# Kernel optimization log

Hardware: AMD Instinct MI355X
Metric: run time of the kernel (lower is better)

The kernel has to match this reference:

```python
import jax, jax.numpy as jnp
import numpy as np

HID = 5120      # hidden_size
QLR = 1536      # q_lora_rank
KVLR = 512      # kv_lora_rank
NOPE = 128      # qk_nope_head_dim
ROPE = 64       # qk_rope_head_dim
VDIM = 128      # v_head_dim
H = 32          # num_local_heads
T = 2048        # tokens (single causal prefill, prefix_len=0)
QKD = NOPE + ROPE
SCALE = QKD ** -0.5
EPS = 1e-6
THETA = 10000.0


def rmsnorm(x, w):
    return x * jax.lax.rsqrt(jnp.mean(x * x, axis=-1, keepdims=True) + EPS) * w


def rope_cos_sin(positions):
    inv_freq = 1.0 / (THETA ** (jnp.arange(0, ROPE, 2, dtype=jnp.float32) / ROPE))
    freqs = positions.astype(jnp.float32)[:, None] * inv_freq  # [T, ROPE/2]
    return jnp.cos(freqs), jnp.sin(freqs)


def apply_rope(x, cos, sin):
    # non-neox (interleaved, GPT-J style) rotation on last dim of size ROPE
    x1 = x[..., ::2]
    x2 = x[..., 1::2]
    o1 = x1 * cos - x2 * sin
    o2 = x2 * cos + x1 * sin
    return jnp.stack([o1, o2], axis=-1).reshape(x.shape)


def setup_inputs() -> dict:
    key = jax.random.key(0)
    ks = jax.random.split(key, 10)
    s = 0.02
    return {
        "hidden_states": jax.random.normal(ks[0], (T, HID), jnp.float32),
        "positions": jnp.arange(T, dtype=jnp.int64),
        "w_q_a": jax.random.normal(ks[1], (HID, QLR), jnp.float32) * s,
        "q_a_ln_w": jnp.ones((QLR,), jnp.float32),
        "w_q_b": jax.random.normal(ks[2], (QLR, H * QKD), jnp.float32) * s,
        "w_kv_a": jax.random.normal(ks[3], (HID, KVLR + ROPE), jnp.float32) * s,
        "kv_a_ln_w": jnp.ones((KVLR,), jnp.float32),
        "w_kc": jax.random.normal(ks[4], (H, NOPE, KVLR), jnp.float32) * s,  # absorbed K weight
        "w_vc": jax.random.normal(ks[5], (H, KVLR, VDIM), jnp.float32) * s,  # absorbed V weight
        "w_o": jax.random.normal(ks[6], (H * VDIM, HID), jnp.float32) * s,
    }


def reference(hidden_states, positions, w_q_a, q_a_ln_w, w_q_b, w_kv_a, kv_a_ln_w, w_kc, w_vc, w_o):
    # --- low-rank Q projection ---
    q = rmsnorm(hidden_states @ w_q_a, q_a_ln_w) @ w_q_b          # [T, H*QKD]
    q = q.reshape(T, H, QKD)
    q_nope, q_pe = q[..., :NOPE], q[..., NOPE:]                   # [T,H,NOPE], [T,H,ROPE]

    # --- absorbed q_nope: project into kv_lora space via w_kc ---
    q_nope_out = jnp.einsum("thd,hdk->thk", q_nope, w_kc)         # [T, H, KVLR]

    # --- latent KV ---
    latent = hidden_states @ w_kv_a                               # [T, KVLR+ROPE]
    v_input = rmsnorm(latent[:, :KVLR], kv_a_ln_w)                # [T, KVLR]
    k_pe = latent[:, KVLR:]                                       # [T, ROPE]

    # --- partial RoPE (non-neox) ---
    cos, sin = rope_cos_sin(positions)                            # [T, ROPE/2]
    q_pe = apply_rope(q_pe, cos[:, None, :], sin[:, None, :])
    k_pe = apply_rope(k_pe, cos, sin)

    q_input = jnp.concatenate([q_nope_out, q_pe], axis=-1)        # [T, H, KVLR+ROPE]
    k_input = jnp.concatenate([v_input, k_pe], axis=-1)           # [T, KVLR+ROPE], shared (MQA)

    # --- causal MQA attention over latent KV ---
    scores = jnp.einsum("thd,sd->hts", q_input, k_input) * SCALE  # [H, T, T]
    causal = jnp.tril(jnp.ones((T, T), dtype=bool))
    scores = jnp.where(causal, scores, -1e30)
    probs = jax.nn.softmax(scores, axis=-1)
    ctx = jnp.einsum("hts,sr->thr", probs, v_input)               # [T, H, KVLR]

    # --- absorbed output projection via w_vc, then o_proj ---
    attn_out = jnp.einsum("thr,hrv->thv", ctx, w_vc).reshape(T, H * VDIM)
    return attn_out @ w_o                                         # [T, HID]
```

## Files before the change

### kernel.cpp

```cpp
#include <hip/hip_runtime.h>

#define T_SEQ 2048
#define HID   5120
#define QLR   1536
#define KVLR  512
#define NOPE  128
#define ROPE_D 64
#define VDIM  128
#define NH    32
#define QKD   192

constexpr float SCALE   = 0.07216878364870323f;
constexpr float EPS_F   = 1e-6f;
constexpr float LN10000 = 9.210340371976184f;

typedef __bf16 bf16x8 __attribute__((ext_vector_type(8)));
typedef float  f32x4  __attribute__((ext_vector_type(4)));

__device__ __forceinline__ unsigned short f2bf(float f) {
  union { float f; unsigned u; } v; v.f = f;
  unsigned u = v.u + 0x7fffu + ((v.u >> 16) & 1u);
  return (unsigned short)(u >> 16);
}
__device__ __forceinline__ float bf2f(unsigned short b) {
  union { unsigned u; float f; } v; v.u = ((unsigned)b) << 16;
  return v.f;
}

__device__ __forceinline__ void glds16(const unsigned short* g, unsigned short* l) {
  __builtin_amdgcn_global_load_lds((const __attribute__((address_space(1))) void*)g,
                                   (__attribute__((address_space(3))) void*)l, 16, 0, 0);
}

__global__ void conv_f2b(const float* __restrict__ in, unsigned short* __restrict__ out, long n) {
  long i = ((long)blockIdx.x * blockDim.x + threadIdx.x) * 4;
  if (i >= n) return;
  float4 v = *(const float4*)(in + i);
  uint2 o;
  o.x = (unsigned)f2bf(v.x) | ((unsigned)f2bf(v.y) << 16);
  o.y = (unsigned)f2bf(v.z) | ((unsigned)f2bf(v.w) << 16);
  *(uint2*)(out + i) = o;
}

__global__ void transpose_f2b(const float* __restrict__ in, unsigned short* __restrict__ out,
                              int R, int C, long inB, long outB) {
  __shared__ float tile[32][33];
  const float* inp = in + (long)blockIdx.z * inB;
  unsigned short* outp = out + (long)blockIdx.z * outB;
  int c0 = blockIdx.x * 32, r0 = blockIdx.y * 32;
  int x = threadIdx.x, y = threadIdx.y;
#pragma unroll
  for (int yy = 0; yy < 32; yy += 8)
    tile[y + yy][x] = inp[(long)(r0 + y + yy) * C + c0 + x];
  __syncthreads();
#pragma unroll
  for (int yy = 0; yy < 32; yy += 8)
    outp[(long)(c0 + y + yy) * R + r0 + x] = f2bf(tile[x][y + yy]);
}

__global__ void rmsnorm_rows(const float* __restrict__ in, const float* __restrict__ w,
                             unsigned short* __restrict__ out, int C) {
  int t = blockIdx.x, tid = threadIdx.x;
  __shared__ float sred[4];
  const float* row = in + (long)t * C;
  float ss = 0.f;
  for (int i = tid; i < C; i += 256) { float v = row[i]; ss += v * v; }
#pragma unroll
  for (int o = 32; o; o >>= 1) ss += __shfl_xor(ss, o);
  if ((tid & 63) == 0) sred[tid >> 6] = ss;
  __syncthreads();
  ss = sred[0] + sred[1] + sred[2] + sred[3];
  float rinv = rsqrtf(ss / (float)C + EPS_F);
  for (int i = tid; i < C; i += 256)
    out[(long)t * C + i] = f2bf(row[i] * rinv * w[i]);
}

__global__ void norm_rope_k(const float* __restrict__ latent, const float* __restrict__ w,
                            unsigned short* __restrict__ k_input, unsigned short* __restrict__ v_t) {
  int t = blockIdx.x, tid = threadIdx.x;
  __shared__ float sred[4];
  const float* row = latent + (long)t * 576;
  float ss = 0.f;
  for (int i = tid; i < 512; i += 256) { float v = row[i]; ss += v * v; }
#pragma unroll
  for (int o = 32; o; o >>= 1) ss += __shfl_xor(ss, o);
  if ((tid & 63) == 0) sred[tid >> 6] = ss;
  __syncthreads();
  ss = sred[0] + sred[1] + sred[2] + sred[3];
  float rinv = rsqrtf(ss * (1.f / 512.f) + EPS_F);
  for (int i = tid; i < 512; i += 256) {
    unsigned short b = f2bf(row[i] * rinv * w[i]);
    k_input[(long)t * 576 + i] = b;
    v_t[(long)i * T_SEQ + t] = b;
  }
  if (tid < 32) {
    float fr = (float)t * expf(-((float)(2 * tid) / 64.f) * LN10000);
    float c = cosf(fr), s = sinf(fr);
    float x1 = row[512 + 2 * tid], x2 = row[512 + 2 * tid + 1];
    k_input[(long)t * 576 + 512 + 2 * tid]     = f2bf(x1 * c - x2 * s);
    k_input[(long)t * 576 + 512 + 2 * tid + 1] = f2bf(x2 * c + x1 * s);
  }
}

__global__ void rope_q(const unsigned short* __restrict__ q, unsigned short* __restrict__ q_input) {
  int idx = blockIdx.x * 256 + threadIdx.x;
  int i = idx & 31, h = (idx >> 5) & 31, t = idx >> 10;
  float fr = (float)t * expf(-((float)(2 * i) / 64.f) * LN10000);
  float c = cosf(fr), s = sinf(fr);
  const unsigned short* qp = q + (long)t * (NH * QKD) + h * QKD + NOPE + 2 * i;
  float x1 = bf2f(qp[0]), x2 = bf2f(qp[1]);
  unsigned short* op = q_input + ((long)h * T_SEQ + t) * 576 + 512 + 2 * i;
  op[0] = f2bf(x1 * c - x2 * s);
  op[1] = f2bf(x2 * c + x1 * s);
}

template <bool OUT_BF16>
__global__ __launch_bounds__(256, 2)
void gemm_bt(const unsigned short* __restrict__ A, const unsigned short* __restrict__ Bt,
             void* __restrict__ Cv, int N, int K,
             long lda, long ldb, long ldc, long bA, long bB, long bC) {
  __shared__ __align__(16) unsigned short sA[128 * 64];
  __shared__ __align__(16) unsigned short sB[128 * 64];
  const int b = blockIdx.z;
  const unsigned short* Ap = A + (long)b * bA;
  const unsigned short* Bp = Bt + (long)b * bB;
  const int m0 = blockIdx.x * 128, n0 = blockIdx.y * 128;
  const int tid = threadIdx.x, lane = tid & 63, w = tid >> 6;
  const int wr = w >> 1, wc = w & 1, lo = lane & 15, hi = lane >> 4;
  f32x4 acc[4][4];
#pragma unroll
  for (int i = 0; i < 4; i++)
#pragma unroll
    for (int j = 0; j < 4; j++) acc[i][j] = (f32x4){0.f, 0.f, 0.f, 0.f};
  const int r0 = tid >> 3, cc = tid & 7;
  for (int k0 = 0; k0 < K; k0 += 64) {
    __syncthreads();
#pragma unroll
    for (int i = 0; i < 4; i++) {
      glds16(Ap + (long)(m0 + i * 32 + r0) * lda + k0 + cc * 8, sA + i * 2048 + w * 512);
      glds16(Bp + (long)(n0 + i * 32 + r0) * ldb + k0 + cc * 8, sB + i * 2048 + w * 512);
    }
    __syncthreads();
#pragma unroll
    for (int s = 0; s < 2; s++) {
      bf16x8 af[4], bfr[4];
#pragma unroll
      for (int mt = 0; mt < 4; mt++)
        af[mt] = *(const bf16x8*)(sA + (wr * 64 + mt * 16 + lo) * 64 + s * 32 + hi * 8);
#pragma unroll
      for (int nt = 0; nt < 4; nt++)
        bfr[nt] = *(const bf16x8*)(sB + (wc * 64 + nt * 16 + lo) * 64 + s * 32 + hi * 8);
#pragma unroll
      for (int mt = 0; mt < 4; mt++)
#pragma unroll
        for (int nt = 0; nt < 4; nt++)
          acc[mt][nt] = __builtin_amdgcn_mfma_f32_16x16x32_bf16(af[mt], bfr[nt], acc[mt][nt], 0, 0, 0);
    }
  }
#pragma unroll
  for (int mt = 0; mt < 4; mt++)
#pragma unroll
    for (int nt = 0; nt < 4; nt++) {
      int col = n0 + wc * 64 + nt * 16 + lo;
      if (col < N) {
#pragma unroll
        for (int r = 0; r < 4; r++) {
          long row = m0 + wr * 64 + mt * 16 + hi * 4 + r;
          float v = acc[mt][nt][r];
          if constexpr (OUT_BF16)
            ((unsigned short*)Cv)[(long)b * bC + row * ldc + col] = f2bf(v);
          else
            ((float*)Cv)[(long)b * bC + row * ldc + col] = v;
        }
      }
    }
}

__global__ __launch_bounds__(256, 2)
void flash_attn(const unsigned short* __restrict__ q_input,
                const unsigned short* __restrict__ k_input,
                const unsigned short* __restrict__ v_t,
                unsigned short* __restrict__ ctx_out) {
  __shared__ __align__(16) unsigned short sK[2 * 64 * 96];
  __shared__ __align__(16) unsigned short sV[2 * 128 * 64];
  const int h = blockIdx.x;
  const int i0 = (31 - blockIdx.y) * 64;
  const int tid = threadIdx.x;
  const int lane = tid & 63, w = tid >> 6;
  const int lo = lane & 15, hi = lane >> 4;
  const int qrow = i0 + w * 16 + lo;

  bf16x8 qf[18];
  {
    const unsigned short* qr = q_input + ((long)h * T_SEQ + qrow) * 576;
#pragma unroll
    for (int i = 0; i < 18; i++) qf[i] = *(const bf16x8*)(qr + i * 32 + hi * 8);
  }
  float l_r = 0.f;
  f32x4 of[32];
#pragma unroll
  for (int o = 0; o < 32; o++) of[o] = (f32x4){0.f, 0.f, 0.f, 0.f};

  int kOff[3];
#pragma unroll
  for (int i = 0; i < 3; i++) {
    int u = w * 192 + i * 64 + lane;
    int key = (u * 683) >> 13;
    int dg = u - 12 * key;
    kOff[i] = key * 576 + dg * 8;
  }
  int vOff[4];
#pragma unroll
  for (int i = 0; i < 4; i++) {
    int u = w * 256 + i * 64 + lane;
    int us = u ^ ((u >> 3) & 7);
    vOff[i] = (u >> 3) * T_SEQ + (us & 7) * 8;
  }
  const int vsw[2] = { ((0 + hi) ^ (lo & 7)) * 8, ((4 + hi) ^ (lo & 7)) * 8 };
  unsigned short* kdst = sK + w * 3 * 512;
  unsigned short* vdst = sV + w * 4 * 512;
  const unsigned short* kld = sK + lo * 96 + hi * 8;
  const unsigned short* vld = sV + lo * 64;

#pragma unroll
  for (int i = 0; i < 3; i++) glds16(k_input + kOff[i], kdst + i * 512);

  for (int j0 = 0; j0 <= i0; j0 += 64) {
    f32x4 sacc[4];
#pragma unroll
    for (int nt = 0; nt < 4; nt++) sacc[nt] = (f32x4){0.f, 0.f, 0.f, 0.f};
#pragma unroll
    for (int c = 0; c < 6; c++) {
      __syncthreads();
      if (c < 5) {
        const int bn = (c + 1) & 1;
#pragma unroll
        for (int i = 0; i < 3; i++)
          glds16(k_input + kOff[i] + (c + 1) * 96, kdst + bn * 6144 + i * 512);
      } else {
#pragma unroll
        for (int i = 0; i < 4; i++) glds16(v_t + vOff[i], vdst + i * 512);
      }
      const unsigned short* kb = kld + (c & 1) * 6144;
#pragma unroll
      for (int ks = 0; ks < 3; ks++)
#pragma unroll
        for (int nt = 0; nt < 4; nt++) {
          bf16x8 a = *(const bf16x8*)(kb + nt * 1536 + ks * 32);
          sacc[nt] = __builtin_amdgcn_mfma_f32_16x16x32_bf16(a, qf[3 * c + ks], sacc[nt], 0, 0, 0);
        }
    }
    const bool diag = (j0 == i0);
    int D2[4][2];
    float psum = 0.f;
#pragma unroll
    for (int nt = 0; nt < 4; nt++) {
      float pv[4];
#pragma unroll
      for (int r = 0; r < 4; r++) {
        float e = __expf(sacc[nt][r] * SCALE);
        if (diag && (j0 + nt * 16 + hi * 4 + r) > qrow) e = 0.f;
        pv[r] = e;
        psum += e;
      }
      D2[nt][0] = (int)f2bf(pv[0]) | ((int)f2bf(pv[1]) << 16);
      D2[nt][1] = (int)f2bf(pv[2]) | ((int)f2bf(pv[3]) << 16);
    }
    psum += __shfl_xor(psum, 16);
    psum += __shfl_xor(psum, 32);
    l_r += psum;
    bf16x8 pa[2];
    {
      const int s0 = lo + 32 * (hi & 1);
#pragma unroll
      for (int kk = 0; kk < 2; kk++) {
        int d[4];
#pragma unroll
        for (int dd = 0; dd < 2; dd++) {
          int t0 = __shfl(D2[2 * kk][dd], s0);
          int t1 = __shfl(D2[2 * kk + 1][dd], s0);
          d[dd] = (hi >> 1) ? t1 : t0;
          int t2 = __shfl(D2[2 * kk][dd], s0 + 16);
          int t3 = __shfl(D2[2 * kk + 1][dd], s0 + 16);
          d[2 + dd] = (hi >> 1) ? t3 : t2;
        }
        int4 di = {d[0], d[1], d[2], d[3]};
        pa[kk] = *(bf16x8*)&di;
      }
    }
#pragma unroll
    for (int ch = 0; ch < 4; ch++) {
      __syncthreads();
      if (ch < 3) {
        const int bn = (ch + 1) & 1;
#pragma unroll
        for (int i = 0; i < 4; i++)
          glds16(v_t + vOff[i] + (ch + 1) * 128 * T_SEQ, vdst + bn * 8192 + i * 512);
      } else {
#pragma unroll
        for (int i = 0; i < 3; i++) kOff[i] += 64 * 576;
#pragma unroll
        for (int i = 0; i < 4; i++) vOff[i] += 64;
        if (j0 < i0) {
#pragma unroll
          for (int i = 0; i < 3; i++) glds16(k_input + kOff[i], kdst + i * 512);
        }
      }
      const unsigned short* vb = vld + (ch & 1) * 8192;
#pragma unroll
      for (int kk = 0; kk < 2; kk++)
#pragma unroll
        for (int ot = 0; ot < 8; ot++) {
          bf16x8 bfr = *(const bf16x8*)(vb + ot * 1024 + vsw[kk]);
          of[ch * 8 + ot] =
              __builtin_amdgcn_mfma_f32_16x16x32_bf16(pa[kk], bfr, of[ch * 8 + ot], 0, 0, 0);
        }
    }
  }
  float linv[4];
#pragma unroll
  for (int r = 0; r < 4; r++) linv[r] = 1.f / __shfl(l_r, hi * 4 + r);
#pragma unroll
  for (int o = 0; o < 32; o++) {
    int vd = (o >> 3) * 128 + (o & 7) * 16 + lo;
#pragma unroll
    for (int r = 0; r < 4; r++) {
      long row = (long)h * T_SEQ + i0 + w * 16 + hi * 4 + r;
      ctx_out[row * 576 + vd] = f2bf(of[o][r] * linv[r]);
    }
  }
}

extern "C" void kernel_launch(void* const* d_in, const int* in_sizes, int n_in,
                              void* d_out, int out_size, void* d_ws, size_t ws_size,
                              hipStream_t stream) {
  (void)in_sizes; (void)n_in; (void)out_size; (void)ws_size;
  const float* hs    = (const float*)d_in[0];
  const float* wqa   = (const float*)d_in[2];
  const float* qlnw  = (const float*)d_in[3];
  const float* wqb   = (const float*)d_in[4];
  const float* wkva  = (const float*)d_in[5];
  const float* kvlnw = (const float*)d_in[6];
  const float* wkc   = (const float*)d_in[7];
  const float* wvc   = (const float*)d_in[8];
  const float* wo    = (const float*)d_in[9];
  float* out = (float*)d_out;

  char* base = (char*)d_ws;
  size_t off = 0;
  auto alloc = [&](size_t bytes) {
    char* r = base + off;
    off += (bytes + 255) & ~(size_t)255;
    return r;
  };
  unsigned short* hs_b  = (unsigned short*)alloc((size_t)T_SEQ * HID * 2);
  unsigned short* wqaT  = (unsigned short*)alloc((size_t)QLR * HID * 2);
  unsigned short* wqbT  = (unsigned short*)alloc((size_t)NH * QKD * QLR * 2);
  unsigned short* wkvaT = (unsigned short*)alloc((size_t)640 * HID * 2);
  unsigned short* wkcT  = (unsigned short*)alloc((size_t)NH * 512 * 128 * 2);
  unsigned short* wvcT  = (unsigned short*)alloc((size_t)NH * 128 * 512 * 2);
  float*          q_a   = (float*)alloc((size_t)T_SEQ * QLR * 4);
  unsigned short* q_a_n = (unsigned short*)alloc((size_t)T_SEQ * QLR * 2);
  unsigned short* qbuf  = (unsigned short*)alloc((size_t)T_SEQ * NH * QKD * 2);
  float*          latent= (float*)alloc((size_t)T_SEQ * 576 * 4);
  unsigned short* k_inp = (unsigned short*)alloc((size_t)T_SEQ * 576 * 2);
  unsigned short* v_t   = (unsigned short*)alloc((size_t)512 * T_SEQ * 2);
  unsigned short* q_inp = (unsigned short*)alloc((size_t)NH * T_SEQ * 576 * 2);
  unsigned short* woT   = (unsigned short*)base;
  unsigned short* attn  = qbuf;

  dim3 tb(32, 8);
  conv_f2b<<<(T_SEQ * HID) / 1024, 256, 0, stream>>>(hs, hs_b, (long)T_SEQ * HID);
  transpose_f2b<<<dim3(QLR / 32, HID / 32, 1), tb, 0, stream>>>(wqa, wqaT, HID, QLR, 0, 0);
  transpose_f2b<<<dim3(576 / 32, HID / 32, 1), tb, 0, stream>>>(wkva, wkvaT, HID, 576, 0, 0);
  gemm_bt<false><<<dim3(T_SEQ / 128, QLR / 128, 1), 256, 0, stream>>>(
      hs_b, wqaT, q_a, QLR, HID, HID, HID, QLR, 0, 0, 0);
  gemm_bt<false><<<dim3(T_SEQ / 128, 5, 1), 256, 0, stream>>>(
      hs_b, wkvaT, latent, 576, HID, HID, HID, 576, 0, 0, 0);
  rmsnorm_rows<<<T_SEQ, 256, 0, stream>>>(q_a, qlnw, q_a_n, QLR);
  norm_rope_k<<<T_SEQ, 256, 0, stream>>>(latent, kvlnw, k_inp, v_t);
  transpose_f2b<<<dim3((NH * QKD) / 32, QLR / 32, 1), tb, 0, stream>>>(wqb, wqbT, QLR, NH * QKD, 0, 0);
  gemm_bt<true><<<dim3(T_SEQ / 128, (NH * QKD) / 128, 1), 256, 0, stream>>>(
      q_a_n, wqbT, qbuf, NH * QKD, QLR, QLR, QLR, NH * QKD, 0, 0, 0);
  transpose_f2b<<<dim3(512 / 32, 128 / 32, NH), tb, 0, stream>>>(wkc, wkcT, 128, 512, 65536, 65536);
  gemm_bt<true><<<dim3(T_SEQ / 128, 512 / 128, NH), 256, 0, stream>>>(
      qbuf, wkcT, q_inp, 512, 128, NH * QKD, 128, 576, QKD, 65536, (long)T_SEQ * 576);
  rope_q<<<(T_SEQ * NH * 32) / 256, 256, 0, stream>>>(qbuf, q_inp);
  flash_attn<<<dim3(NH, 32), 256, 0, stream>>>(q_inp, k_inp, v_t, q_inp);
  transpose_f2b<<<dim3(128 / 32, 512 / 32, NH), tb, 0, stream>>>(wvc, wvcT, 512, 128, 65536, 65536);
  gemm_bt<true><<<dim3(T_SEQ / 128, 1, NH), 256, 0, stream>>>(
      q_inp, wvcT, attn, 128, 512, 576, 512, NH * VDIM, (long)T_SEQ * 576, 65536, 128);
  transpose_f2b<<<dim3(HID / 32, (NH * VDIM) / 32, 1), tb, 0, stream>>>(wo, woT, NH * VDIM, HID, 0, 0);
  gemm_bt<false><<<dim3(T_SEQ / 128, HID / 128, 1), 256, 0, stream>>>(
      attn, woT, out, HID, NH * VDIM, NH * VDIM, NH * VDIM, HID, 0, 0, 0);
}
```

Measured before the change: 1.075 ms.

## Deepen flash-attention K/V staging to a 4-buffer pipeline with explicit vmcnt waits

```diff
diff --git a/kernel.cpp b/kernel.cpp
--- a/kernel.cpp
+++ b/kernel.cpp
@@ -181,8 +181,8 @@
                 const unsigned short* __restrict__ k_input,
                 const unsigned short* __restrict__ v_t,
                 unsigned short* __restrict__ ctx_out) {
-  __shared__ __align__(16) unsigned short sK[2 * 64 * 96];
-  __shared__ __align__(16) unsigned short sV[2 * 128 * 64];
+  __shared__ __align__(16) unsigned short sK[4 * 64 * 64];
+  __shared__ __align__(16) unsigned short sV[4 * 64 * 64];
   const int h = blockIdx.x;
   const int i0 = (31 - blockIdx.y) * 64;
   const int tid = threadIdx.x;
@@ -196,60 +196,92 @@
 #pragma unroll
     for (int i = 0; i < 18; i++) qf[i] = *(const bf16x8*)(qr + i * 32 + hi * 8);
   }
+#pragma unroll
+  for (int i = 0; i < 18; i++) asm volatile("" : "+v"(qf[i]));
+
   float l_r = 0.f;
   f32x4 of[32];
 #pragma unroll
   for (int o = 0; o < 32; o++) of[o] = (f32x4){0.f, 0.f, 0.f, 0.f};
 
-  int kOff[3];
-#pragma unroll
-  for (int i = 0; i < 3; i++) {
-    int u = w * 192 + i * 64 + lane;
-    int key = (u * 683) >> 13;
-    int dg = u - 12 * key;
-    kOff[i] = key * 576 + dg * 8;
-  }
-  int vOff[4];
-#pragma unroll
-  for (int i = 0; i < 4; i++) {
-    int u = w * 256 + i * 64 + lane;
-    int us = u ^ ((u >> 3) & 7);
-    vOff[i] = (u >> 3) * T_SEQ + (us & 7) * 8;
-  }
-  const int vsw[2] = { ((0 + hi) ^ (lo & 7)) * 8, ((4 + hi) ^ (lo & 7)) * 8 };
-  unsigned short* kdst = sK + w * 3 * 512;
-  unsigned short* vdst = sV + w * 4 * 512;
-  const unsigned short* kld = sK + lo * 96 + hi * 8;
+  int kOff[2], vOff[2];
+#pragma unroll
+  for (int i = 0; i < 2; i++) {
+    int u = w * 128 + i * 64 + lane;
+    int sl = (u ^ (u >> 3)) & 7;
+    kOff[i] = (u >> 3) * 576 + sl * 8;
+    vOff[i] = (u >> 3) * T_SEQ + sl * 8;
+  }
+  const int sw[2] = { ((0 + hi) ^ (lo & 7)) * 8, ((4 + hi) ^ (lo & 7)) * 8 };
+  unsigned short* kdst = sK + w * 1024;
+  unsigned short* vdst = sV + w * 1024;
+  const unsigned short* kld = sK + lo * 64;
   const unsigned short* vld = sV + lo * 64;
 
-#pragma unroll
-  for (int i = 0; i < 3; i++) glds16(k_input + kOff[i], kdst + i * 512);
+#define STAGE_K(c, base)                                                      \
+  {                                                                           \
+    unsigned short* d_ = kdst + ((c) & 3) * 4096;                             \
+    _Pragma("unroll")                                                         \
+    for (int i_ = 0; i_ < 2; i_++)                                            \
+      glds16(k_input + (base) + kOff[i_] + (c) * 64, d_ + i_ * 512);          \
+  }
+#define STAGE_V(ch, jk)                                                       \
+  {                                                                           \
+    unsigned short* d_ = vdst + ((ch) & 3) * 4096;                            \
+    _Pragma("unroll")                                                         \
+    for (int i_ = 0; i_ < 2; i_++)                                            \
+      glds16(v_t + (long)(ch) * 64 * T_SEQ + vOff[i_] + (jk), d_ + i_ * 512); \
+  }
+#define WB(N)                                                                 \
+  __builtin_amdgcn_sched_barrier(0);                                          \
+  asm volatile("s_waitcnt vmcnt(" #N ")" ::: "memory");                       \
+  __builtin_amdgcn_s_barrier();                                               \
+  __builtin_amdgcn_sched_barrier(0);
+#define COMPUTE_K(c)                                                          \
+  {                                                                           \
+    const unsigned short* kb_ = kld + ((c) & 3) * 4096;                       \
+    _Pragma("unroll")                                                         \
+    for (int ks_ = 0; ks_ < 2; ks_++)                                         \
+      _Pragma("unroll")                                                       \
+      for (int nt_ = 0; nt_ < 4; nt_++) {                                     \
+        bf16x8 a_ = *(const bf16x8*)(kb_ + nt_ * 1024 + sw[ks_]);             \
+        sacc[nt_] = __builtin_amdgcn_mfma_f32_16x16x32_bf16(                  \
+            a_, qf[2 * (c) + ks_], sacc[nt_], 0, 0, 0);                       \
+      }                                                                       \
+  }
+#define COMPUTE_V(ch)                                                         \
+  {                                                                           \
+    const unsigned short* vb_ = vld + ((ch) & 3) * 4096;                      \
+    _Pragma("unroll")                                                         \
+    for (int kk_ = 0; kk_ < 2; kk_++)                                         \
+      _Pragma("unroll")                                                       \
+      for (int ot_ = 0; ot_ < 4; ot_++) {                                     \
+        bf16x8 b_ = *(const bf16x8*)(vb_ + ot_ * 1024 + sw[kk_]);             \
+        of[(ch) * 4 + ot_] = __builtin_amdgcn_mfma_f32_16x16x32_bf16(         \
+            pa[kk_], b_, of[(ch) * 4 + ot_], 0, 0, 0);                        \
+      }                                                                       \
+  }
+
+  STAGE_K(0, 0); STAGE_K(1, 0);
 
   for (int j0 = 0; j0 <= i0; j0 += 64) {
+    const long kcur = (long)j0 * 576;
+    const long knxt = kcur + 64 * 576;
+    const bool more = (j0 < i0);
     f32x4 sacc[4];
 #pragma unroll
     for (int nt = 0; nt < 4; nt++) sacc[nt] = (f32x4){0.f, 0.f, 0.f, 0.f};
-#pragma unroll
-    for (int c = 0; c < 6; c++) {
-      __syncthreads();
-      if (c < 5) {
-        const int bn = (c + 1) & 1;
-#pragma unroll
-        for (int i = 0; i < 3; i++)
-          glds16(k_input + kOff[i] + (c + 1) * 96, kdst + bn * 6144 + i * 512);
-      } else {
-#pragma unroll
-        for (int i = 0; i < 4; i++) glds16(v_t + vOff[i], vdst + i * 512);
-      }
-      const unsigned short* kb = kld + (c & 1) * 6144;
-#pragma unroll
-      for (int ks = 0; ks < 3; ks++)
-#pragma unroll
-        for (int nt = 0; nt < 4; nt++) {
-          bf16x8 a = *(const bf16x8*)(kb + nt * 1536 + ks * 32);
-          sacc[nt] = __builtin_amdgcn_mfma_f32_16x16x32_bf16(a, qf[3 * c + ks], sacc[nt], 0, 0, 0);
-        }
-    }
+
+    STAGE_K(2, kcur); WB(4); COMPUTE_K(0);
+    STAGE_K(3, kcur); WB(4); COMPUTE_K(1);
+    STAGE_K(4, kcur); WB(4); COMPUTE_K(2);
+    STAGE_K(5, kcur); WB(4); COMPUTE_K(3);
+    STAGE_K(6, kcur); WB(4); COMPUTE_K(4);
+    STAGE_K(7, kcur); WB(4); COMPUTE_K(5);
+    STAGE_K(8, kcur); WB(4); COMPUTE_K(6);
+    STAGE_V(0, j0);   WB(4); COMPUTE_K(7);
+    STAGE_V(1, j0);   WB(4); COMPUTE_K(8);
+
     const bool diag = (j0 == i0);
     int D2[4][2];
     float psum = 0.f;
@@ -288,41 +320,29 @@
         pa[kk] = *(bf16x8*)&di;
       }
     }
-#pragma unroll
-    for (int ch = 0; ch < 4; ch++) {
-      __syncthreads();
-      if (ch < 3) {
-        const int bn = (ch + 1) & 1;
-#pragma unroll
-        for (int i = 0; i < 4; i++)
-          glds16(v_t + vOff[i] + (ch + 1) * 128 * T_SEQ, vdst + bn * 8192 + i * 512);
-      } else {
-#pragma unroll
-        for (int i = 0; i < 3; i++) kOff[i] += 64 * 576;
-#pragma unroll
-        for (int i = 0; i < 4; i++) vOff[i] += 64;
-        if (j0 < i0) {
-#pragma unroll
-          for (int i = 0; i < 3; i++) glds16(k_input + kOff[i], kdst + i * 512);
-        }
-      }
-      const unsigned short* vb = vld + (ch & 1) * 8192;
-#pragma unroll
-      for (int kk = 0; kk < 2; kk++)
-#pragma unroll
-        for (int ot = 0; ot < 8; ot++) {
-          bf16x8 bfr = *(const bf16x8*)(vb + ot * 1024 + vsw[kk]);
-          of[ch * 8 + ot] =
-              __builtin_amdgcn_mfma_f32_16x16x32_bf16(pa[kk], bfr, of[ch * 8 + ot], 0, 0, 0);
-        }
-    }
-  }
+    STAGE_V(2, j0); WB(4); COMPUTE_V(0);
+    STAGE_V(3, j0); WB(4); COMPUTE_V(1);
+    STAGE_V(4, j0); WB(4); COMPUTE_V(2);
+    STAGE_V(5, j0); WB(4); COMPUTE_V(3);
+    STAGE_V(6, j0); WB(4); COMPUTE_V(4);
+    STAGE_V(7, j0); WB(4); COMPUTE_V(5);
+    if (more) { STAGE_K(0, knxt); WB(4); } else { WB(2); }
+    COMPUTE_V(6);
+    if (more) { STAGE_K(1, knxt); WB(4); } else { WB(0); }
+    COMPUTE_V(7);
+  }
+#undef STAGE_K
+#undef STAGE_V
+#undef WB
+#undef COMPUTE_K
+#undef COMPUTE_V
+
   float linv[4];
 #pragma unroll
   for (int r = 0; r < 4; r++) linv[r] = 1.f / __shfl(l_r, hi * 4 + r);
 #pragma unroll
   for (int o = 0; o < 32; o++) {
-    int vd = (o >> 3) * 128 + (o & 7) * 16 + lo;
+    int vd = o * 16 + lo;
 #pragma unroll
     for (int r = 0; r < 4; r++) {
       long row = (long)h * T_SEQ + i0 + w * 16 + hi * 4 + r;
```

New measurement: 992.3 us. 7.7% less time.
